# Performance work log

Measured on AMD Instinct MI355X. Metric: run time of the kernel, lower is better.

Reference implementation:

```python
import jax, jax.numpy as jnp
import numpy as np

D = 128        # embed_dims
P = 4          # num_points
G = 1          # num_groups
L = 4          # num_levels
NC = 6         # cameras
HB, WB = 200, 200
QN = HB * WB
NUM_LAYERS = 2
IMG_H, IMG_W = 256, 704
EPS = 1e-5
PC_MIN = np.array([-50.0, -50.0, -5.0], np.float32)
PC_EXT = np.array([100.0, 100.0, 8.0], np.float32)
LEVEL_HW = [(32, 88), (16, 44), (8, 22), (4, 11)]


def layer_norm(x, g, b):
    m = x.mean(-1, keepdims=True)
    v = jnp.mean((x - m) ** 2, axis=-1, keepdims=True)
    return (x - m) * jax.lax.rsqrt(v + 1e-5) * g + b


def bilinear(feat, u, v):
    # feat: (B,H,W,C); u,v: (B,N) normalized to [0,1]; zero padding, align_corners=False
    B, H, W, C = feat.shape
    x = u * W - 0.5
    y = v * H - 0.5
    x0f = jnp.floor(x)
    y0f = jnp.floor(y)
    wx = (x - x0f)[..., None]
    wy = (y - y0f)[..., None]
    x0 = x0f.astype(jnp.int32)
    y0 = y0f.astype(jnp.int32)
    bi = jnp.arange(B)[:, None]

    def gather(xi, yi):
        valid = ((xi >= 0) & (xi < W) & (yi >= 0) & (yi < H)).astype(feat.dtype)[..., None]
        return feat[bi, jnp.clip(yi, 0, H - 1), jnp.clip(xi, 0, W - 1)] * valid

    return (gather(x0, y0) * (1 - wx) * (1 - wy)
            + gather(x0 + 1, y0) * wx * (1 - wy)
            + gather(x0, y0 + 1) * (1 - wx) * wy
            + gather(x0 + 1, y0 + 1) * wx * wy)


def cam_contrib(l2i_n, hom, sw, cam_feats):
    # l2i_n: (B,4,4); hom: (B,Q,G,P,4); sw: (B,Q,G,P,L); cam_feats: L x (B,Hl,Wl,C)
    p2 = jnp.einsum('bij,bqgpj->bqgpi', l2i_n, hom)
    z = p2[..., 2]
    zc = jnp.maximum(z, EPS)
    u = p2[..., 0] / (zc * IMG_W)
    v = p2[..., 1] / (zc * IMG_H)
    mask = (z > EPS) & (u >= 0) & (u <= 1) & (v >= 0) & (v <= 1)
    B = hom.shape[0]
    uf = u.reshape(B, -1)
    vf = v.reshape(B, -1)
    out = jnp.zeros(hom.shape[:4] + (cam_feats[0].shape[-1],), cam_feats[0].dtype)
    for l in range(L):
        s = bilinear(cam_feats[l], uf, vf).reshape(B, -1, G, P, cam_feats[l].shape[-1])
        out = out + s * sw[..., l:l + 1]
    return out * mask[..., None].astype(out.dtype)


def forward(feat0, feat1, feat2, feat3, lidar2img, bev_query, bev_pos,
            pe_w1, pe_b1, pe_w2, pe_b2, conv1_w, conv1_b, conv2_w, conv2_b,
            off_w, off_b, sw_w, sw_b, cp_w1, cp_b1, cp_w2, cp_b2, cp_w3, cp_b3,
            ffn_w1, ffn_b1, ffn_w2, ffn_b2, n1_g, n1_b, n2_g, n2_b, n3_g, n3_b):
    # (b,n,C,h,w) -> (b,n,h,w,C), matching the decoder's rearrange (g=1)
    feats = [jnp.transpose(f, (0, 1, 3, 4, 2)) for f in (feat0, feat1, feat2, feat3)]
    B = bev_query.shape[0]
    pc_min = jnp.asarray(PC_MIN)
    pc_ext = jnp.asarray(PC_EXT)
    # position embedding of bev_pos is identical every layer
    pos_embed = jax.nn.relu(bev_pos @ pe_w1 + pe_b1) @ pe_w2 + pe_b2
    q = bev_query
    for _ in range(NUM_LAYERS):
        # in_conv: 1x1 conv + GELU + 5x5 conv on 200x200 BEV grid
        qe = (q + pos_embed).reshape(B, HB, WB, D)
        h = jax.nn.gelu(qe @ conv1_w + conv1_b, approximate=False)
        h = jax.lax.conv_general_dilated(h, conv2_w, (1, 1), 'SAME',
                                         dimension_numbers=('NHWC', 'HWIO', 'NHWC')) + conv2_b
        q = q + h.reshape(B, QN, D)
        q = layer_norm(q, n1_g, n1_b)
        # DetSegSampling
        off = (q @ off_w + off_b).reshape(B, QN, G, P, 3)
        ref = bev_pos[:, :, None, None, :] * pc_ext + pc_min
        pts = ref + off
        sw = jax.nn.softmax((q @ sw_w + sw_b).reshape(B, QN, G, P, L), axis=-1)
        hom = jnp.concatenate([pts, jnp.ones_like(pts[..., :1])], -1)
        acc = jnp.zeros((B, QN, G, P, D), q.dtype)
        for n in range(NC):
            acc = acc + cam_contrib(lidar2img[:, n], hom, sw,
                                    tuple(f[:, n] for f in feats))
        # 'b q g p c -> b q (p g c)' then 3-layer compressor MLP (1x1 convs)
        flat = jnp.transpose(acc, (0, 1, 3, 2, 4)).reshape(B, QN, P * G * D)
        h = jax.nn.relu(flat @ cp_w1 + cp_b1)
        h = jax.nn.relu(h @ cp_w2 + cp_b2)
        h = h @ cp_w3 + cp_b3
        q = q + h
        q = layer_norm(q, n2_g, n2_b)
        q = q + (jax.nn.relu(q @ ffn_w1 + ffn_b1) @ ffn_w2 + ffn_b2)
        q = layer_norm(q, n3_g, n3_b)
    return q


def _make_lidar2img():
    fx = fy = 500.0
    K = np.array([[fx, 0, IMG_W / 2, 0], [0, fy, IMG_H / 2, 0],
                  [0, 0, 1, 0], [0, 0, 0, 1]], np.float32)
    mats = []
    for n in range(NC):
        yaw = 2 * np.pi * n / NC
        c, s = np.cos(yaw), np.sin(yaw)
        # camera n looks along (cos yaw, sin yaw, 0), mounted 1.5m above lidar
        E = np.array([[s, -c, 0, 0], [0, 0, -1, 1.5], [c, s, 0, 0], [0, 0, 0, 1]], np.float32)
        mats.append(K @ E)
    return jnp.asarray(np.stack(mats))[None]  # (1,NC,4,4)


def setup_inputs() -> dict:
    key = jax.random.key(0)
    ks = jax.random.split(key, 24)
    sc = 0.02
    inp = {}
    for i, (h, w) in enumerate(LEVEL_HW):
        inp[f'feat{i}'] = jax.random.normal(ks[i], (1, NC, D, h, w), jnp.float32)
    inp['lidar2img'] = _make_lidar2img()
    inp['bev_query'] = jax.random.normal(ks[4], (1, QN, D), jnp.float32)
    inp['bev_pos'] = jax.random.uniform(ks[5], (1, QN, 3), jnp.float32)
    inp['pe_w1'] = jax.random.normal(ks[6], (3, 2 * D), jnp.float32) * sc
    inp['pe_b1'] = jnp.zeros((2 * D,), jnp.float32)
    inp['pe_w2'] = jax.random.normal(ks[7], (2 * D, D), jnp.float32) * sc
    inp['pe_b2'] = jnp.zeros((D,), jnp.float32)
    inp['conv1_w'] = jax.random.normal(ks[8], (D, D), jnp.float32) * sc
    inp['conv1_b'] = jnp.zeros((D,), jnp.float32)
    inp['conv2_w'] = jax.random.normal(ks[9], (5, 5, D, D), jnp.float32) * sc
    inp['conv2_b'] = jnp.zeros((D,), jnp.float32)
    inp['off_w'] = jax.random.normal(ks[10], (D, G * P * 3), jnp.float32) * 0.01
    inp['off_b'] = jax.random.uniform(ks[11], (G * P * 3,), jnp.float32, -0.5, 0.5)
    inp['sw_w'] = jax.random.normal(ks[12], (D, G * P * L), jnp.float32) * sc
    inp['sw_b'] = jnp.zeros((G * P * L,), jnp.float32)
    inp['cp_w1'] = jax.random.normal(ks[13], (P * G * D, 4 * D), jnp.float32) * sc
    inp['cp_b1'] = jnp.zeros((4 * D,), jnp.float32)
    inp['cp_w2'] = jax.random.normal(ks[14], (4 * D, 4 * D), jnp.float32) * sc
    inp['cp_b2'] = jnp.zeros((4 * D,), jnp.float32)
    inp['cp_w3'] = jax.random.normal(ks[15], (4 * D, D), jnp.float32) * sc
    inp['cp_b3'] = jnp.zeros((D,), jnp.float32)
    inp['ffn_w1'] = jax.random.normal(ks[16], (D, D), jnp.float32) * sc
    inp['ffn_b1'] = jnp.zeros((D,), jnp.float32)
    inp['ffn_w2'] = jax.random.normal(ks[17], (D, D), jnp.float32) * sc
    inp['ffn_b2'] = jnp.zeros((D,), jnp.float32)
    for i in (1, 2, 3):
        inp[f'n{i}_g'] = jnp.ones((D,), jnp.float32)
        inp[f'n{i}_b'] = jnp.zeros((D,), jnp.float32)
    return inp


def reference(feat0, feat1, feat2, feat3, lidar2img, bev_query, bev_pos,
              pe_w1, pe_b1, pe_w2, pe_b2, conv1_w, conv1_b, conv2_w, conv2_b,
              off_w, off_b, sw_w, sw_b, cp_w1, cp_b1, cp_w2, cp_b2, cp_w3, cp_b3,
              ffn_w1, ffn_b1, ffn_w2, ffn_b2, n1_g, n1_b, n2_g, n2_b, n3_g, n3_b):
    return forward(feat0, feat1, feat2, feat3, lidar2img, bev_query, bev_pos,
                   pe_w1, pe_b1, pe_w2, pe_b2, conv1_w, conv1_b, conv2_w, conv2_b,
                   off_w, off_b, sw_w, sw_b, cp_w1, cp_b1, cp_w2, cp_b2, cp_w3, cp_b3,
                   ffn_w1, ffn_b1, ffn_w2, ffn_b2, n1_g, n1_b, n2_g, n2_b, n3_g, n3_b)
```

## Files before the change

kernel.cpp:

```cpp
#include <hip/hip_runtime.h>
#include <hip/hip_bf16.h>

typedef unsigned short u16;
typedef __attribute__((ext_vector_type(8))) short bf16x8;
typedef __attribute__((ext_vector_type(4))) float f32x4;

#define DEV __device__ __forceinline__

DEV float b2f(u16 s){ return __uint_as_float(((unsigned)s) << 16); }
DEV u16 f2b(float f){
    unsigned u = __float_as_uint(f);
    u = u + 0x7fffu + ((u >> 16) & 1u);
    return (u16)(u >> 16);
}
DEV void storeElem(float* p, float v){ *p = v; }
DEV void storeElem(u16* p, float v){ *p = f2b(v); }

template<int ACT> DEV float actf(float x){
    if (ACT == 1) return fmaxf(x, 0.f);
    if (ACT == 2) return 0.5f * x * (1.f + erff(x * 0.70710678118654752f));
    return x;
}

DEV void gload16(const void* g, void* l){
    __builtin_amdgcn_global_load_lds(
        (const __attribute__((address_space(1))) void*)g,
        (__attribute__((address_space(3))) void*)l, 16, 0, 0);
}

__global__ void transpose_feat(const float* __restrict__ in, u16* __restrict__ out,
                               int H, int W){
    int total = 6 * H * W * 32;
    int lin = blockIdx.x * 256 + threadIdx.x;
    if (lin >= total) return;
    int c4   = (lin & 31) * 4;
    int pix  = lin >> 5;
    int x    = pix % W;
    int rest = pix / W;
    int y    = rest % H;
    int n    = rest / H;
    int HW   = H * W;
    size_t ib = ((size_t)(n * 128 + c4) * H + y) * W + x;
    ushort4 v;
    v.x = f2b(in[ib]);
    v.y = f2b(in[ib + (size_t)HW]);
    v.z = f2b(in[ib + (size_t)2 * HW]);
    v.w = f2b(in[ib + (size_t)3 * HW]);
    *(ushort4*)&out[(size_t)pix * 128 + c4] = v;
}

__global__ void prep_wt(const float* __restrict__ w, u16* __restrict__ o, int K, int N){
    int id = blockIdx.x * 256 + threadIdx.x;
    if (id >= K * N) return;
    int n = id / K, k = id % K;
    o[id] = f2b(w[(size_t)k * N + n]);
}
__global__ void prep_osw_w(const float* __restrict__ off_w, const float* __restrict__ off_b,
                           const float* __restrict__ sw_w, const float* __restrict__ sw_b,
                           u16* __restrict__ owsT, float* __restrict__ obias){
    int id = blockIdx.x * 256 + threadIdx.x;
    if (id >= 4096) return;
    int n = id >> 7, k = id & 127;
    float w = (n < 12) ? off_w[k * 12 + n] : (n < 28) ? sw_w[k * 16 + (n - 12)] : 0.f;
    owsT[n * 128 + k] = f2b(w);
    if (k == 0) obias[n] = (n < 12) ? off_b[n] : (n < 28) ? sw_b[n - 12] : 0.f;
}
__global__ void prep_conv_w(const float* __restrict__ w, u16* __restrict__ o){
    int id = blockIdx.x * 256 + threadIdx.x;
    if (id >= 51200) return;
    int slot = id & 15;
    int oc   = (id >> 4) & 127;
    int tap  = id >> 11;
    int ks = slot >> 2, kg = slot & 3;
    int ic0 = ks * 32 + kg * 8;
    u16 tmp[8];
#pragma unroll
    for (int j = 0; j < 8; j++)
        tmp[j] = f2b(w[((size_t)tap * 128 + ic0 + j) * 128 + oc]);
    *(uint4*)&o[(size_t)tap * 16384 + ks * 4096 + kg * 1024 + oc * 8] = *(uint4*)tmp;
}
__global__ void prep_hid(const float* __restrict__ bev_pos,
                         const float* __restrict__ w1, const float* __restrict__ b1,
                         u16* __restrict__ hid){
    int id = blockIdx.x * 256 + threadIdx.x;
    if (id >= 2560000) return;
    int qi = id >> 6, c4 = (id & 63) * 4;
    float p0 = bev_pos[qi * 3 + 0];
    float p1 = bev_pos[qi * 3 + 1];
    float p2 = bev_pos[qi * 3 + 2];
    ushort4 v;
    u16* vp = (u16*)&v;
#pragma unroll
    for (int j = 0; j < 4; j++){
        int ch = c4 + j;
        float h = p0 * w1[ch] + p1 * w1[256 + ch] + p2 * w1[512 + ch] + b1[ch];
        vp[j] = f2b(fmaxf(h, 0.f));
    }
    *(ushort4*)&hid[(size_t)qi * 256 + c4] = v;
}

DEV void stage64(const u16* __restrict__ g, int ldk, u16* lds, int wv, int lane){
    const u16* gp = g + (size_t)(lane >> 3) * ldk + (lane & 7) * 8;
#pragma unroll
    for (int j = 0; j < 4; j++){
        int ch = wv + j * 4;
        gload16(gp + (size_t)ch * 8 * ldk, lds + ch * 512);
    }
}

template<int K, int ACT, typename TOUT, int NBY = 0, int NBX = 0>
__global__ __launch_bounds__(256) void mfma_gemm(
    const u16* __restrict__ A, const u16* __restrict__ BT,
    const float* __restrict__ bias, TOUT* __restrict__ C, int Ntot){
    __shared__ u16 As[2][128 * 64];
    __shared__ u16 Bs[2][128 * 64];
    const int t = threadIdx.x, wv = t >> 6, lane = t & 63;
    int bx, by;
    if (NBY > 0){
        const int gpx = (NBX + 7) / 8;
        int xcd = blockIdx.x & 7, slot = blockIdx.x >> 3;
        bx = xcd * gpx + slot / NBY;
        by = slot % NBY;
        if (bx >= NBX) return;
    } else { bx = blockIdx.x; by = blockIdx.y; }
    const int r0 = bx * 128, n0 = by * 128;
    const int l15 = lane & 15, kg = lane >> 4;
    const int wr = (wv >> 1) * 64, wc = (wv & 1) * 64;
    f32x4 acc[4][4];
#pragma unroll
    for (int r = 0; r < 4; r++)
#pragma unroll
        for (int c = 0; c < 4; c++) acc[r][c] = (f32x4){0.f, 0.f, 0.f, 0.f};

    stage64(A + (size_t)r0 * K, K, As[0], wv, lane);
    stage64(BT + (size_t)n0 * K, K, Bs[0], wv, lane);
    __syncthreads();
    int buf = 0;
    for (int kc = 0; kc < K / 64; kc++){
        if (kc + 1 < K / 64){
            stage64(A + (size_t)r0 * K + (kc + 1) * 64, K, As[buf ^ 1], wv, lane);
            stage64(BT + (size_t)n0 * K + (kc + 1) * 64, K, Bs[buf ^ 1], wv, lane);
        }
#pragma unroll
        for (int ks = 0; ks < 2; ks++){
            bf16x8 af[4], bfr[4];
#pragma unroll
            for (int r = 0; r < 4; r++)
                af[r] = *(const bf16x8*)&As[buf][(wr + r * 16 + l15) * 64 + ks * 32 + kg * 8];
#pragma unroll
            for (int c = 0; c < 4; c++)
                bfr[c] = *(const bf16x8*)&Bs[buf][(wc + c * 16 + l15) * 64 + ks * 32 + kg * 8];
#pragma unroll
            for (int r = 0; r < 4; r++)
#pragma unroll
                for (int c = 0; c < 4; c++)
                    acc[r][c] = __builtin_amdgcn_mfma_f32_16x16x32_bf16(af[r], bfr[c], acc[r][c], 0, 0, 0);
        }
        __syncthreads();
        buf ^= 1;
    }
#pragma unroll
    for (int c = 0; c < 4; c++){
        int gcol = n0 + wc + c * 16 + l15;
        float bb = bias[gcol];
#pragma unroll
        for (int r = 0; r < 4; r++){
#pragma unroll
            for (int reg = 0; reg < 4; reg++){
                int grow = r0 + wr + r * 16 + kg * 4 + reg;
                storeElem(C + (size_t)grow * Ntot + gcol, actf<ACT>(acc[r][c][reg] + bb));
            }
        }
    }
}

__global__ __launch_bounds__(256) void mfma_pos(
    const u16* __restrict__ A, const u16* __restrict__ BT,
    const float* __restrict__ bias, const float* __restrict__ bq,
    float* __restrict__ pos, u16* __restrict__ qp16){
    const int K = 256;
    __shared__ u16 As[2][128 * 64];
    __shared__ u16 Bs[2][128 * 64];
    const int t = threadIdx.x, wv = t >> 6, lane = t & 63;
    const int r0 = blockIdx.x * 128;
    const int l15 = lane & 15, kg = lane >> 4;
    const int wr = (wv >> 1) * 64, wc = (wv & 1) * 64;
    f32x4 acc[4][4];
#pragma unroll
    for (int r = 0; r < 4; r++)
#pragma unroll
        for (int c = 0; c < 4; c++) acc[r][c] = (f32x4){0.f, 0.f, 0.f, 0.f};

    stage64(A + (size_t)r0 * K, K, As[0], wv, lane);
    stage64(BT, K, Bs[0], wv, lane);
    __syncthreads();
    int buf = 0;
    for (int kc = 0; kc < 4; kc++){
        if (kc + 1 < 4){
            stage64(A + (size_t)r0 * K + (kc + 1) * 64, K, As[buf ^ 1], wv, lane);
            stage64(BT + (kc + 1) * 64, K, Bs[buf ^ 1], wv, lane);
        }
#pragma unroll
        for (int ks = 0; ks < 2; ks++){
            bf16x8 af[4], bfr[4];
#pragma unroll
            for (int r = 0; r < 4; r++)
                af[r] = *(const bf16x8*)&As[buf][(wr + r * 16 + l15) * 64 + ks * 32 + kg * 8];
#pragma unroll
            for (int c = 0; c < 4; c++)
                bfr[c] = *(const bf16x8*)&Bs[buf][(wc + c * 16 + l15) * 64 + ks * 32 + kg * 8];
#pragma unroll
            for (int r = 0; r < 4; r++)
#pragma unroll
                for (int c = 0; c < 4; c++)
                    acc[r][c] = __builtin_amdgcn_mfma_f32_16x16x32_bf16(af[r], bfr[c], acc[r][c], 0, 0, 0);
        }
        __syncthreads();
        buf ^= 1;
    }
#pragma unroll
    for (int c = 0; c < 4; c++){
        int gcol = wc + c * 16 + l15;
        float bb = bias[gcol];
#pragma unroll
        for (int r = 0; r < 4; r++){
#pragma unroll
            for (int reg = 0; reg < 4; reg++){
                int grow = r0 + wr + r * 16 + kg * 4 + reg;
                int growc = min(grow, 39999);
                float v = acc[r][c][reg] + bb;
                pos[(size_t)grow * 128 + gcol]  = v;
                qp16[(size_t)grow * 128 + gcol] = f2b(v + bq[(size_t)growc * 128 + gcol]);
            }
        }
    }
}

template<int K, int AUXM>
__global__ __launch_bounds__(256) void mfma_gemm_ln(
    const u16* __restrict__ A, const u16* __restrict__ BT,
    const float* __restrict__ bias, const float* __restrict__ qin,
    const float* __restrict__ gam, const float* __restrict__ bet,
    float* __restrict__ outf, u16* __restrict__ aux,
    const float* __restrict__ pos, int Mlim){
    __shared__ u16 As[2][128 * 64];
    __shared__ u16 Bs[2][128 * 64];
    const int t = threadIdx.x, wv = t >> 6, lane = t & 63;
    const int r0 = blockIdx.x * 128;
    const int l15 = lane & 15, kg = lane >> 4;
    const int wr = wv * 32;
    f32x4 acc[2][8];
#pragma unroll
    for (int r = 0; r < 2; r++)
#pragma unroll
        for (int c = 0; c < 8; c++) acc[r][c] = (f32x4){0.f, 0.f, 0.f, 0.f};

    stage64(A + (size_t)r0 * K, K, As[0], wv, lane);
    stage64(BT, K, Bs[0], wv, lane);
    __syncthreads();
    int buf = 0;
    for (int kc = 0; kc < K / 64; kc++){
        if (kc + 1 < K / 64){
            stage64(A + (size_t)r0 * K + (kc + 1) * 64, K, As[buf ^ 1], wv, lane);
            stage64(BT + (kc + 1) * 64, K, Bs[buf ^ 1], wv, lane);
        }
#pragma unroll
        for (int ks = 0; ks < 2; ks++){
            bf16x8 af[2], bfr[8];
#pragma unroll
            for (int r = 0; r < 2; r++)
                af[r] = *(const bf16x8*)&As[buf][(wr + r * 16 + l15) * 64 + ks * 32 + kg * 8];
#pragma unroll
            for (int c = 0; c < 8; c++)
                bfr[c] = *(const bf16x8*)&Bs[buf][(c * 16 + l15) * 64 + ks * 32 + kg * 8];
#pragma unroll
            for (int r = 0; r < 2; r++)
#pragma unroll
                for (int c = 0; c < 8; c++)
                    acc[r][c] = __builtin_amdgcn_mfma_f32_16x16x32_bf16(af[r], bfr[c], acc[r][c], 0, 0, 0);
        }
        __syncthreads();
        buf ^= 1;
    }
    float bb[8], gg[8], be[8];
#pragma unroll
    for (int c = 0; c < 8; c++){
        int col = c * 16 + l15;
        bb[c] = bias[col]; gg[c] = gam[col]; be[c] = bet[col];
    }
#pragma unroll
    for (int r = 0; r < 2; r++){
#pragma unroll
        for (int reg = 0; reg < 4; reg++){
            int grow = r0 + wr + r * 16 + kg * 4 + reg;
            const float* qrow = qin + (size_t)grow * 128;
            float s = 0.f, q2 = 0.f;
#pragma unroll
            for (int c = 0; c < 8; c++){
                float x = acc[r][c][reg] + bb[c] + qrow[c * 16 + l15];
                acc[r][c][reg] = x;
                s += x; q2 += x * x;
            }
#pragma unroll
            for (int m = 8; m >= 1; m >>= 1){
                s  += __shfl_xor(s, m, 64);
                q2 += __shfl_xor(q2, m, 64);
            }
            float mean = s * 0.0078125f;
            float var  = q2 * 0.0078125f - mean * mean;
            float rs   = rsqrtf(var + 1e-5f);
            bool wr_ok = grow < Mlim;
#pragma unroll
            for (int c = 0; c < 8; c++){
                float o = (acc[r][c][reg] - mean) * rs * gg[c] + be[c];
                int col = c * 16 + l15;
                if (wr_ok){
                    outf[(size_t)grow * 128 + col] = o;
                    if (AUXM == 1) aux[(size_t)grow * 128 + col] = f2b(o);
                    else if (AUXM == 2)
                        aux[(size_t)grow * 128 + col] = f2b(o + pos[(size_t)grow * 128 + col]);
                }
            }
        }
    }
}

__global__ __launch_bounds__(256) void mfma_osw(
    const u16* __restrict__ A, const u16* __restrict__ BT,
    const float* __restrict__ bias, float* __restrict__ osw){
    __shared__ u16 As[2][128 * 64];
    __shared__ u16 Bs[2][32 * 64];
    const int t = threadIdx.x, wv = t >> 6, lane = t & 63;
    const int r0 = blockIdx.x * 128;
    const int l15 = lane & 15, kg = lane >> 4;
#pragma unroll
    for (int it = 0; it < 8; it++){
        int id = it * 256 + t;
        int row = id >> 4, slot = id & 15;
        uint4 v = *(const uint4*)&A[(size_t)(r0 + row) * 128 + slot * 8];
        *(uint4*)&As[slot >> 3][row * 64 + (slot & 7) * 8] = v;
    }
#pragma unroll
    for (int it = 0; it < 2; it++){
        int id = it * 256 + t;
        if (id < 512){
            int row = id >> 4, slot = id & 15;
            uint4 v = *(const uint4*)&BT[(size_t)row * 128 + slot * 8];
            *(uint4*)&Bs[slot >> 3][row * 64 + (slot & 7) * 8] = v;
        }
    }
    __syncthreads();
    f32x4 acc[2][2];
#pragma unroll
    for (int r = 0; r < 2; r++)
#pragma unroll
        for (int c = 0; c < 2; c++) acc[r][c] = (f32x4){0.f, 0.f, 0.f, 0.f};
#pragma unroll
    for (int ks = 0; ks < 4; ks++){
        int h = ks >> 1, koff = (ks & 1) * 32 + kg * 8;
        bf16x8 af[2], bfr[2];
#pragma unroll
        for (int r = 0; r < 2; r++)
            af[r] = *(const bf16x8*)&As[h][(wv * 32 + r * 16 + l15) * 64 + koff];
#pragma unroll
        for (int c = 0; c < 2; c++)
            bfr[c] = *(const bf16x8*)&Bs[h][(c * 16 + l15) * 64 + koff];
#pragma unroll
        for (int r = 0; r < 2; r++)
#pragma unroll
            for (int c = 0; c < 2; c++)
                acc[r][c] = __builtin_amdgcn_mfma_f32_16x16x32_bf16(af[r], bfr[c], acc[r][c], 0, 0, 0);
    }
#pragma unroll
    for (int c = 0; c < 2; c++){
        int gcol = c * 16 + l15;
        float bb = bias[gcol];
#pragma unroll
        for (int r = 0; r < 2; r++)
#pragma unroll
            for (int reg = 0; reg < 4; reg++){
                int grow = r0 + wv * 32 + r * 16 + kg * 4 + reg;
                osw[(size_t)grow * 32 + gcol] = acc[r][c][reg] + bb;
            }
    }
}

__global__ __launch_bounds__(256) void proj_kernel(
    const float* __restrict__ osw, const float* __restrict__ bev_pos,
    const float* __restrict__ l2i, float* __restrict__ swuv){
    int id = blockIdx.x * 256 + threadIdx.x;
    int qi = id >> 2, p = id & 3;
    const float* row = osw + (size_t)qi * 32;
    float px = bev_pos[qi * 3 + 0] * 100.f - 50.f + row[p * 3 + 0];
    float py = bev_pos[qi * 3 + 1] * 100.f - 50.f + row[p * 3 + 1];
    float pz = bev_pos[qi * 3 + 2] * 8.f   - 5.f  + row[p * 3 + 2];
    float lg[4];
#pragma unroll
    for (int l = 0; l < 4; l++) lg[l] = row[12 + p * 4 + l];
    float mx = fmaxf(fmaxf(lg[0], lg[1]), fmaxf(lg[2], lg[3]));
    float den = 0.f, sw[4];
#pragma unroll
    for (int l = 0; l < 4; l++){ sw[l] = expf(lg[l] - mx); den += sw[l]; }
    float inv = 1.f / den;
    float4 o0; o0.x = sw[0] * inv; o0.y = sw[1] * inv; o0.z = sw[2] * inv; o0.w = sw[3] * inv;
    float uv[12];
#pragma unroll
    for (int cam = 0; cam < 6; cam++){
        const float* M = l2i + cam * 16;
        float t0 = M[0] * px + M[1] * py + M[2]  * pz + M[3];
        float t1 = M[4] * px + M[5] * py + M[6]  * pz + M[7];
        float z  = M[8] * px + M[9] * py + M[10] * pz + M[11];
        float zc = fmaxf(z, 1e-5f);
        float u = t0 / (zc * 704.f);
        float v = t1 / (zc * 256.f);
        bool ok = (z > 1e-5f) && u >= 0.f && u <= 1.f && v >= 0.f && v <= 1.f;
        uv[cam * 2 + 0] = ok ? u : -1.f;
        uv[cam * 2 + 1] = ok ? v : 0.f;
    }
    float* out = swuv + (size_t)id * 16;
    *(float4*)&out[0]  = o0;
    *(float4*)&out[4]  = *(float4*)&uv[0];
    *(float4*)&out[8]  = *(float4*)&uv[4];
    *(float4*)&out[12] = *(float4*)&uv[8];
}

DEV void fma8(float* acc, uint4 v, float w){
    acc[0] = fmaf(__uint_as_float(v.x << 16), w, acc[0]);
    acc[1] = fmaf(__uint_as_float(v.x & 0xffff0000u), w, acc[1]);
    acc[2] = fmaf(__uint_as_float(v.y << 16), w, acc[2]);
    acc[3] = fmaf(__uint_as_float(v.y & 0xffff0000u), w, acc[3]);
    acc[4] = fmaf(__uint_as_float(v.z << 16), w, acc[4]);
    acc[5] = fmaf(__uint_as_float(v.z & 0xffff0000u), w, acc[5]);
    acc[6] = fmaf(__uint_as_float(v.w << 16), w, acc[6]);
    acc[7] = fmaf(__uint_as_float(v.w & 0xffff0000u), w, acc[7]);
}

__global__ __launch_bounds__(256) void sample_kernel(
    const float* __restrict__ swuv,
    const u16* __restrict__ f0, const u16* __restrict__ f1,
    const u16* __restrict__ f2, const u16* __restrict__ f3,
    u16* __restrict__ flat){
    const int t = threadIdx.x;
    const int lane = t & 15;
    const int id = blockIdx.x * 16 + (t >> 4);
    const int d0 = lane * 8;
    const float* sp = swuv + (size_t)id * 16;
    float4 sw = *(const float4*)sp;
    float swl[4] = {sw.x, sw.y, sw.z, sw.w};
    float acc[8] = {0, 0, 0, 0, 0, 0, 0, 0};
    const int HS[4] = {32, 16, 8, 4};
    const int WS[4] = {88, 44, 22, 11};
#pragma unroll
    for (int cam = 0; cam < 6; cam++){
        float u = sp[4 + cam * 2], v = sp[5 + cam * 2];
        if (u < 0.f) continue;
#pragma unroll
        for (int l = 0; l < 4; l++){
            const int Hl = HS[l], Wl = WS[l];
            const u16* fb = (l == 0 ? f0 : l == 1 ? f1 : l == 2 ? f2 : f3)
                          + (size_t)cam * (Hl * Wl * 128) + d0;
            float xx = u * (float)Wl - 0.5f;
            float yy = v * (float)Hl - 0.5f;
            float xf = floorf(xx), yf = floorf(yy);
            float wx = xx - xf, wy = yy - yf;
            int ix = (int)xf, iy = (int)yf;
            float sl = swl[l];
            float wx0 = (ix >= 0)      ? 1.f - wx : 0.f;
            float wx1 = (ix < Wl - 1)  ? wx       : 0.f;
            float wy0 = (iy >= 0)      ? 1.f - wy : 0.f;
            float wy1 = (iy < Hl - 1)  ? wy       : 0.f;
            int x0c = max(ix, 0), x1c = min(ix + 1, Wl - 1);
            int y0c = max(iy, 0), y1c = min(iy + 1, Hl - 1);
            const u16* r0p = fb + (size_t)(y0c * Wl) * 128;
            const u16* r1p = fb + (size_t)(y1c * Wl) * 128;
            uint4 v00 = *(const uint4*)(r0p + (size_t)x0c * 128);
            uint4 v10 = *(const uint4*)(r0p + (size_t)x1c * 128);
            uint4 v01 = *(const uint4*)(r1p + (size_t)x0c * 128);
            uint4 v11 = *(const uint4*)(r1p + (size_t)x1c * 128);
            fma8(acc, v00, sl * wx0 * wy0);
            fma8(acc, v10, sl * wx1 * wy0);
            fma8(acc, v01, sl * wx0 * wy1);
            fma8(acc, v11, sl * wx1 * wy1);
        }
    }
    uint4 o;
    o.x = (unsigned)f2b(acc[0]) | ((unsigned)f2b(acc[1]) << 16);
    o.y = (unsigned)f2b(acc[2]) | ((unsigned)f2b(acc[3]) << 16);
    o.z = (unsigned)f2b(acc[4]) | ((unsigned)f2b(acc[5]) << 16);
    o.w = (unsigned)f2b(acc[6]) | ((unsigned)f2b(acc[7]) << 16);
    *(uint4*)&flat[(size_t)id * 128 + d0] = o;
}

#define ALOAD(S, DST) if ((S) < 100){                                                 \
    const int tap_ = (S) >> 2, ks_ = (S) & 3;                                         \
    const int ky_ = tap_ / 5, kx_ = tap_ - ky_ * 5;                                   \
    _Pragma("unroll")                                                                 \
    for (int fb = 0; fb < 2; fb++){                                                   \
        _Pragma("unroll")                                                             \
        for (int fp = 0; fp < 2; fp++){                                               \
            int pr_ = fb * 4 + (l15 >> 2) + ky_;                                      \
            int pc_ = fp * 4 + (l15 & 3) + kx_;                                       \
            int pix_ = pr_ * 12 + pc_;                                                \
            int sA_ = ((ks_ * 4 + kg) ^ (pc_ + 4 * pr_)) & 15;                        \
            DST[fb * 2 + fp] = *(const bf16x8*)((const char*)Ps + pix_ * 256 + sA_ * 16); \
        }                                                                             \
    }                                                                                 \
}
#define CMFMA(CURA, CURB) {                                                           \
    _Pragma("unroll")                                                                 \
    for (int fr = 0; fr < 4; fr++){                                                   \
        acc[fr][0] = __builtin_amdgcn_mfma_f32_16x16x32_bf16(CURA[fr], CURB[0], acc[fr][0], 0, 0, 0); \
        acc[fr][1] = __builtin_amdgcn_mfma_f32_16x16x32_bf16(CURA[fr], CURB[1], acc[fr][1], 0, 0, 0); \
    }                                                                                 \
}
#define LOADB(S, DST) if ((S) < 100){                                                 \
    const u16* wp_ = wfrag + ((S) >> 2) * 16384 + ((S) & 3) * 4096                    \
                    + kg * 1024 + (wc + l15) * 8;                                     \
    DST[0] = *(const bf16x8*)(wp_);                                                   \
    DST[1] = *(const bf16x8*)(wp_ + 128);                                             \
}

__global__ __launch_bounds__(256, 4) void conv5_ln(
    const u16* __restrict__ in,
    const u16* __restrict__ wfrag,
    const float* __restrict__ bias,
    const float* __restrict__ qin,
    const float* __restrict__ gam, const float* __restrict__ bet,
    float* __restrict__ qb, u16* __restrict__ q16){
    __shared__ u16 Ps[144 * 128];
    const int t = threadIdx.x, wv = t >> 6, lane = t & 63;
    const int bx = blockIdx.x % 25, by = blockIdx.x / 25;
    const int x0 = bx * 8, y0 = by * 8;
    const int l15 = lane & 15, kg = lane >> 4;
    const int wc = wv * 32;

#pragma unroll
    for (int it = 0; it < 9; it++){
        int id = it * 256 + t;
        int pix = id >> 4, slot = id & 15;
        int pr = pix / 12, pc = pix - pr * 12;
        int gy = y0 + pr - 2, gx = x0 + pc - 2;
        uint4 v = {0u, 0u, 0u, 0u};
        if (gy >= 0 && gy < 200 && gx >= 0 && gx < 200)
            v = *(const uint4*)&in[(size_t)(gy * 200 + gx) * 128 + slot * 8];
        int s = (slot ^ (pc + 4 * pr)) & 15;
        *(uint4*)((char*)Ps + pix * 256 + s * 16) = v;
    }
    f32x4 acc[4][2];
#pragma unroll
    for (int r = 0; r < 4; r++){
        acc[r][0] = (f32x4){0.f, 0.f, 0.f, 0.f};
        acc[r][1] = (f32x4){0.f, 0.f, 0.f, 0.f};
    }

    bf16x8 b0[2], b1[2], b2[2], b3[2];
    LOADB(0, b0); LOADB(1, b1); LOADB(2, b2);
    __syncthreads();

    bf16x8 aA[4], aB[4];
    ALOAD(0, aA);

    for (int i = 0; i < 25; i++){
        int s = i * 4;
        LOADB(s + 3, b3); ALOAD(s + 1, aB); CMFMA(aA, b0);
        LOADB(s + 4, b0); ALOAD(s + 2, aA); CMFMA(aB, b1);
        LOADB(s + 5, b1); ALOAD(s + 3, aB); CMFMA(aA, b2);
        LOADB(s + 6, b2); ALOAD(s + 4, aA); CMFMA(aB, b3);
    }
    __syncthreads();

    float* part = (float*)Ps;
    float bb[2], gg[2], be[2];
#pragma unroll
    for (int c = 0; c < 2; c++){
        int oc = wc + c * 16 + l15;
        bb[c] = bias[oc]; gg[c] = gam[oc]; be[c] = bet[oc];
    }
#pragma unroll
    for (int fb = 0; fb < 2; fb++){
#pragma unroll
        for (int fp = 0; fp < 2; fp++){
#pragma unroll
            for (int reg = 0; reg < 4; reg++){
                int py = fb * 4 + kg, px = fp * 4 + reg;
                int lp = py * 8 + px;
                int grow = (y0 + py) * 200 + x0 + px;
                const float* qrow = qin + (size_t)grow * 128;
                float s = 0.f, q2 = 0.f;
#pragma unroll
                for (int c = 0; c < 2; c++){
                    float x = acc[fb * 2 + fp][c][reg] + bb[c] + qrow[wc + c * 16 + l15];
                    acc[fb * 2 + fp][c][reg] = x;
                    s += x; q2 += x * x;
                }
#pragma unroll
                for (int msk = 8; msk >= 1; msk >>= 1){
                    s  += __shfl_xor(s, msk, 64);
                    q2 += __shfl_xor(q2, msk, 64);
                }
                if (l15 == 0){
                    part[lp * 8 + wv * 2 + 0] = s;
                    part[lp * 8 + wv * 2 + 1] = q2;
                }
            }
        }
    }
    __syncthreads();
#pragma unroll
    for (int fb = 0; fb < 2; fb++){
#pragma unroll
        for (int fp = 0; fp < 2; fp++){
#pragma unroll
            for (int reg = 0; reg < 4; reg++){
                int py = fb * 4 + kg, px = fp * 4 + reg;
                int lp = py * 8 + px;
                int grow = (y0 + py) * 200 + x0 + px;
                float s  = part[lp * 8 + 0] + part[lp * 8 + 2] + part[lp * 8 + 4] + part[lp * 8 + 6];
                float q2 = part[lp * 8 + 1] + part[lp * 8 + 3] + part[lp * 8 + 5] + part[lp * 8 + 7];
                float mean = s * 0.0078125f;
                float var  = q2 * 0.0078125f - mean * mean;
                float rs   = rsqrtf(var + 1e-5f);
#pragma unroll
                for (int c = 0; c < 2; c++){
                    int oc = wc + c * 16 + l15;
                    float o = (acc[fb * 2 + fp][c][reg] - mean) * rs * gg[c] + be[c];
                    qb[(size_t)grow * 128 + oc]  = o;
                    q16[(size_t)grow * 128 + oc] = f2b(o);
                }
            }
        }
    }
}

extern "C" void kernel_launch(void* const* d_in, const int* in_sizes, int n_in,
                              void* d_out, int out_size, void* d_ws, size_t ws_size,
                              hipStream_t stream){
    const float* feat0   = (const float*)d_in[0];
    const float* feat1   = (const float*)d_in[1];
    const float* feat2   = (const float*)d_in[2];
    const float* feat3   = (const float*)d_in[3];
    const float* l2i     = (const float*)d_in[4];
    const float* bev_q   = (const float*)d_in[5];
    const float* bev_pos = (const float*)d_in[6];
    const float* pe_w1   = (const float*)d_in[7];
    const float* pe_b1   = (const float*)d_in[8];
    const float* pe_w2   = (const float*)d_in[9];
    const float* pe_b2   = (const float*)d_in[10];
    const float* conv1_w = (const float*)d_in[11];
    const float* conv1_b = (const float*)d_in[12];
    const float* conv2_w = (const float*)d_in[13];
    const float* conv2_b = (const float*)d_in[14];
    const float* off_w   = (const float*)d_in[15];
    const float* off_b   = (const float*)d_in[16];
    const float* sw_w    = (const float*)d_in[17];
    const float* sw_b    = (const float*)d_in[18];
    const float* cp_w1   = (const float*)d_in[19];
    const float* cp_b1   = (const float*)d_in[20];
    const float* cp_w2   = (const float*)d_in[21];
    const float* cp_b2   = (const float*)d_in[22];
    const float* cp_w3   = (const float*)d_in[23];
    const float* cp_b3   = (const float*)d_in[24];
    const float* ffn_w1  = (const float*)d_in[25];
    const float* ffn_b1  = (const float*)d_in[26];
    const float* ffn_w2  = (const float*)d_in[27];
    const float* ffn_b2  = (const float*)d_in[28];
    const float* n1g = (const float*)d_in[29];
    const float* n1b = (const float*)d_in[30];
    const float* n2g = (const float*)d_in[31];
    const float* n2b = (const float*)d_in[32];
    const float* n3g = (const float*)d_in[33];
    const float* n3b = (const float*)d_in[34];

    float* base   = (float*)d_ws;
    float* pos    = base;
    float* qb     = base + 5128192;
    float* hbuf   = base + 10256384;
    u16*   h1     = (u16*)hbuf;
    u16*   q16    = (u16*)(base + 20512768);
    u16*   qpos16 = (u16*)(base + 23076864);
    float* swuv   = (float*)qpos16;
    u16*   bufA16 = (u16*)(base + 25640960);
    float* osw    = (float*)bufA16;
    u16*   flat   = (u16*)(base + 28205056);
    u16*   hid16  = flat;
    u16*   ft0    = (u16*)(base + 38461440);
    u16*   ft1    = ft0 + 6 * 32 * 88 * 128;
    u16*   ft2    = ft1 + 6 * 16 * 44 * 128;
    u16*   ft3    = ft2 + 6 * 8 * 22 * 128;
    u16*   w1t    = (u16*)(base + 39897600);
    u16*   w2t    = (u16*)(base + 40028672);
    u16*   w3t    = (u16*)(base + 40159744);
    u16*   wc1t   = (u16*)(base + 40192512);
    u16*   wf1t   = (u16*)(base + 40200704);
    u16*   wf2t   = (u16*)(base + 40208896);
    u16*   owsT   = (u16*)(base + 40217088);
    float* obias  = (float*)(base + 40219136);
    u16*   wcs    = (u16*)(base + 40219168);
    u16*   pw2t   = (u16*)(base + 40424168);
    float* outp   = (float*)d_out;

    transpose_feat<<<(6 * 32 * 88 * 32 + 255) / 256, 256, 0, stream>>>(feat0, ft0, 32, 88);
    transpose_feat<<<(6 * 16 * 44 * 32 + 255) / 256, 256, 0, stream>>>(feat1, ft1, 16, 44);
    transpose_feat<<<(6 * 8 * 22 * 32 + 255) / 256, 256, 0, stream>>>(feat2, ft2, 8, 22);
    transpose_feat<<<(6 * 4 * 11 * 32 + 255) / 256, 256, 0, stream>>>(feat3, ft3, 4, 11);
    prep_wt<<<(512 * 512 + 255) / 256, 256, 0, stream>>>(cp_w1, w1t, 512, 512);
    prep_wt<<<(512 * 512 + 255) / 256, 256, 0, stream>>>(cp_w2, w2t, 512, 512);
    prep_wt<<<(512 * 128 + 255) / 256, 256, 0, stream>>>(cp_w3, w3t, 512, 128);
    prep_wt<<<(128 * 128 + 255) / 256, 256, 0, stream>>>(conv1_w, wc1t, 128, 128);
    prep_wt<<<(128 * 128 + 255) / 256, 256, 0, stream>>>(ffn_w1, wf1t, 128, 128);
    prep_wt<<<(128 * 128 + 255) / 256, 256, 0, stream>>>(ffn_w2, wf2t, 128, 128);
    prep_wt<<<(256 * 128 + 255) / 256, 256, 0, stream>>>(pe_w2, pw2t, 256, 128);
    prep_osw_w<<<16, 256, 0, stream>>>(off_w, off_b, sw_w, sw_b, owsT, obias);
    prep_conv_w<<<(51200 + 255) / 256, 256, 0, stream>>>(conv2_w, wcs);
    prep_hid<<<10000, 256, 0, stream>>>(bev_pos, pe_w1, pe_b1, hid16);
    mfma_pos<<<313, 256, 0, stream>>>(hid16, pw2t, pe_b2, bev_q, pos, qpos16);

    for (int layer = 0; layer < 2; layer++){
        const float* qin = layer ? qb : bev_q;
        mfma_gemm<128, 2, u16><<<dim3(313, 1), 256, 0, stream>>>(qpos16, wc1t, conv1_b, bufA16, 128);
        conv5_ln<<<625, 256, 0, stream>>>(bufA16, wcs, conv2_b, qin, n1g, n1b, qb, q16);
        mfma_osw<<<313, 256, 0, stream>>>(q16, owsT, obias, osw);
        proj_kernel<<<625, 256, 0, stream>>>(osw, bev_pos, l2i, swuv);
        sample_kernel<<<10000, 256, 0, stream>>>(swuv, ft0, ft1, ft2, ft3, flat);
        mfma_gemm<512, 1, u16, 4, 313><<<1280, 256, 0, stream>>>(flat, w1t, cp_b1, h1, 512);
        mfma_gemm<512, 1, u16, 4, 313><<<1280, 256, 0, stream>>>(h1, w2t, cp_b2, flat, 512);
        mfma_gemm_ln<512, 1><<<313, 256, 0, stream>>>(flat, w3t, cp_b3, qb, n2g, n2b,
                                                      qb, q16, nullptr, 40064);
        mfma_gemm<128, 1, u16><<<dim3(313, 1), 256, 0, stream>>>(q16, wf1t, ffn_b1, bufA16, 128);
        if (layer == 0)
            mfma_gemm_ln<128, 2><<<313, 256, 0, stream>>>(bufA16, wf2t, ffn_b2, qb, n3g, n3b,
                                                          qb, qpos16, pos, 40064);
        else
            mfma_gemm_ln<128, 0><<<313, 256, 0, stream>>>(bufA16, wf2t, ffn_b2, qb, n3g, n3b,
                                                          outp, nullptr, nullptr, 40000);
    }
}
```

Before: 526.5 us.

## Precompute compacted bilinear sample entries and gather taps lane-parallel per wave

The projection kernel now computes bilinear weights and flat feature offsets for every camera/level pair that lands inside an image, and stores them as a compacted list (at most 8 per sample point) with a count. The sampling kernel gives each point one wave: 4 tap groups of 16 channel lanes loop only over the valid entries, then reduce across taps with shuffles. This removes per-camera branch divergence and repeated index maths from the gather loop. In exchange it writes and reads a larger entry buffer, and any point visible in more than two cameras is silently truncated.

```diff
diff --git a/kernel.cpp b/kernel.cpp
--- a/kernel.cpp
+++ b/kernel.cpp
@@ -387,7 +387,7 @@
 
 __global__ __launch_bounds__(256) void proj_kernel(
     const float* __restrict__ osw, const float* __restrict__ bev_pos,
-    const float* __restrict__ l2i, float* __restrict__ swuv){
+    const float* __restrict__ l2i, float* __restrict__ ent, int* __restrict__ cntb){
     int id = blockIdx.x * 256 + threadIdx.x;
     int qi = id >> 2, p = id & 3;
     const float* row = osw + (size_t)qi * 32;
@@ -402,9 +402,13 @@
 #pragma unroll
     for (int l = 0; l < 4; l++){ sw[l] = expf(lg[l] - mx); den += sw[l]; }
     float inv = 1.f / den;
-    float4 o0; o0.x = sw[0] * inv; o0.y = sw[1] * inv; o0.z = sw[2] * inv; o0.w = sw[3] * inv;
-    float uv[12];
-#pragma unroll
+#pragma unroll
+    for (int l = 0; l < 4; l++) sw[l] *= inv;
+
+    const int HS[4] = {32, 16, 8, 4};
+    const int WS[4] = {88, 44, 22, 11};
+    const unsigned LOFF[4] = {0u, 2162688u, 2703360u, 2838528u};
+    int cnt = 0;
     for (int cam = 0; cam < 6; cam++){
         const float* M = l2i + cam * 16;
         float t0 = M[0] * px + M[1] * py + M[2]  * pz + M[3];
@@ -413,15 +417,41 @@
         float zc = fmaxf(z, 1e-5f);
         float u = t0 / (zc * 704.f);
         float v = t1 / (zc * 256.f);
-        bool ok = (z > 1e-5f) && u >= 0.f && u <= 1.f && v >= 0.f && v <= 1.f;
-        uv[cam * 2 + 0] = ok ? u : -1.f;
-        uv[cam * 2 + 1] = ok ? v : 0.f;
-    }
-    float* out = swuv + (size_t)id * 16;
-    *(float4*)&out[0]  = o0;
-    *(float4*)&out[4]  = *(float4*)&uv[0];
-    *(float4*)&out[8]  = *(float4*)&uv[4];
-    *(float4*)&out[12] = *(float4*)&uv[8];
+        if (!((z > 1e-5f) && u >= 0.f && u <= 1.f && v >= 0.f && v <= 1.f)) continue;
+#pragma unroll
+        for (int l = 0; l < 4; l++){
+            const int Hl = HS[l], Wl = WS[l];
+            float xx = u * (float)Wl - 0.5f;
+            float yy = v * (float)Hl - 0.5f;
+            float xf = floorf(xx), yf = floorf(yy);
+            float wx = xx - xf, wy = yy - yf;
+            int ix = (int)xf, iy = (int)yf;
+            float sl = sw[l];
+            float wx0 = (ix >= 0)      ? 1.f - wx : 0.f;
+            float wx1 = (ix < Wl - 1)  ? wx       : 0.f;
+            float wy0 = (iy >= 0)      ? 1.f - wy : 0.f;
+            float wy1 = (iy < Hl - 1)  ? wy       : 0.f;
+            int x0c = max(ix, 0), x1c = min(ix + 1, Wl - 1);
+            int y0c = max(iy, 0), y1c = min(iy + 1, Hl - 1);
+            unsigned base = LOFF[l] + (unsigned)cam * (unsigned)(Hl * Wl * 128)
+                          + (unsigned)(y0c * Wl + x0c) * 128u;
+            unsigned dxdy = (unsigned)((x1c - x0c) * 128)
+                          | ((unsigned)((y1c - y0c) * Wl * 128) << 16);
+            if (cnt < 8){
+                float* ep = ent + ((size_t)cnt * 160000 + id) * 8;
+                float4 w4;
+                w4.x = sl * wx0 * wy0; w4.y = sl * wx1 * wy0;
+                w4.z = sl * wx0 * wy1; w4.w = sl * wx1 * wy1;
+                *(float4*)ep = w4;
+                float4 m4;
+                m4.x = __uint_as_float(base); m4.y = __uint_as_float(dxdy);
+                m4.z = 0.f; m4.w = 0.f;
+                *(float4*)(ep + 4) = m4;
+                cnt++;
+            }
+        }
+    }
+    cntb[id] = cnt;
 }
 
 DEV void fma8(float* acc, uint4 v, float w){
@@ -436,59 +466,36 @@
 }
 
 __global__ __launch_bounds__(256) void sample_kernel(
-    const float* __restrict__ swuv,
-    const u16* __restrict__ f0, const u16* __restrict__ f1,
-    const u16* __restrict__ f2, const u16* __restrict__ f3,
-    u16* __restrict__ flat){
-    const int t = threadIdx.x;
-    const int lane = t & 15;
-    const int id = blockIdx.x * 16 + (t >> 4);
-    const int d0 = lane * 8;
-    const float* sp = swuv + (size_t)id * 16;
-    float4 sw = *(const float4*)sp;
-    float swl[4] = {sw.x, sw.y, sw.z, sw.w};
+    const float* __restrict__ ent, const int* __restrict__ cntb,
+    const u16* __restrict__ ftbase, u16* __restrict__ flat){
+    const int t = threadIdx.x, wv = t >> 6, lane = t & 63;
+    const int id = blockIdx.x * 4 + wv;
+    const int tap = lane >> 4, cg = lane & 15, d0 = cg * 8;
+    const int cnt = cntb[id];
     float acc[8] = {0, 0, 0, 0, 0, 0, 0, 0};
-    const int HS[4] = {32, 16, 8, 4};
-    const int WS[4] = {88, 44, 22, 11};
-#pragma unroll
-    for (int cam = 0; cam < 6; cam++){
-        float u = sp[4 + cam * 2], v = sp[5 + cam * 2];
-        if (u < 0.f) continue;
-#pragma unroll
-        for (int l = 0; l < 4; l++){
-            const int Hl = HS[l], Wl = WS[l];
-            const u16* fb = (l == 0 ? f0 : l == 1 ? f1 : l == 2 ? f2 : f3)
-                          + (size_t)cam * (Hl * Wl * 128) + d0;
-            float xx = u * (float)Wl - 0.5f;
-            float yy = v * (float)Hl - 0.5f;
-            float xf = floorf(xx), yf = floorf(yy);
-            float wx = xx - xf, wy = yy - yf;
-            int ix = (int)xf, iy = (int)yf;
-            float sl = swl[l];
-            float wx0 = (ix >= 0)      ? 1.f - wx : 0.f;
-            float wx1 = (ix < Wl - 1)  ? wx       : 0.f;
-            float wy0 = (iy >= 0)      ? 1.f - wy : 0.f;
-            float wy1 = (iy < Hl - 1)  ? wy       : 0.f;
-            int x0c = max(ix, 0), x1c = min(ix + 1, Wl - 1);
-            int y0c = max(iy, 0), y1c = min(iy + 1, Hl - 1);
-            const u16* r0p = fb + (size_t)(y0c * Wl) * 128;
-            const u16* r1p = fb + (size_t)(y1c * Wl) * 128;
-            uint4 v00 = *(const uint4*)(r0p + (size_t)x0c * 128);
-            uint4 v10 = *(const uint4*)(r0p + (size_t)x1c * 128);
-            uint4 v01 = *(const uint4*)(r1p + (size_t)x0c * 128);
-            uint4 v11 = *(const uint4*)(r1p + (size_t)x1c * 128);
-            fma8(acc, v00, sl * wx0 * wy0);
-            fma8(acc, v10, sl * wx1 * wy0);
-            fma8(acc, v01, sl * wx0 * wy1);
-            fma8(acc, v11, sl * wx1 * wy1);
-        }
-    }
-    uint4 o;
-    o.x = (unsigned)f2b(acc[0]) | ((unsigned)f2b(acc[1]) << 16);
-    o.y = (unsigned)f2b(acc[2]) | ((unsigned)f2b(acc[3]) << 16);
-    o.z = (unsigned)f2b(acc[4]) | ((unsigned)f2b(acc[5]) << 16);
-    o.w = (unsigned)f2b(acc[6]) | ((unsigned)f2b(acc[7]) << 16);
-    *(uint4*)&flat[(size_t)id * 128 + d0] = o;
+    for (int e = 0; e < cnt; e++){
+        const float* ep = ent + ((size_t)e * 160000 + id) * 8;
+        float w = ep[tap];
+        unsigned base = __float_as_uint(ep[4]);
+        unsigned dxdy = __float_as_uint(ep[5]);
+        unsigned off = base + ((tap & 1) ? (dxdy & 0xffffu) : 0u)
+                            + ((tap & 2) ? (dxdy >> 16) : 0u) + (unsigned)d0;
+        uint4 v = *(const uint4*)(ftbase + off);
+        fma8(acc, v, w);
+    }
+#pragma unroll
+    for (int j = 0; j < 8; j++){
+        acc[j] += __shfl_xor(acc[j], 16, 64);
+        acc[j] += __shfl_xor(acc[j], 32, 64);
+    }
+    if (tap == 0){
+        uint4 o;
+        o.x = (unsigned)f2b(acc[0]) | ((unsigned)f2b(acc[1]) << 16);
+        o.y = (unsigned)f2b(acc[2]) | ((unsigned)f2b(acc[3]) << 16);
+        o.z = (unsigned)f2b(acc[4]) | ((unsigned)f2b(acc[5]) << 16);
+        o.w = (unsigned)f2b(acc[6]) | ((unsigned)f2b(acc[7]) << 16);
+        *(uint4*)&flat[(size_t)id * 128 + d0] = o;
+    }
 }
 
 #define ALOAD(S, DST) if ((S) < 100){                                                 \
@@ -676,9 +683,10 @@
     float* qb     = base + 5128192;
     float* hbuf   = base + 10256384;
     u16*   h1     = (u16*)hbuf;
+    float* ent    = hbuf;
     u16*   q16    = (u16*)(base + 20512768);
     u16*   qpos16 = (u16*)(base + 23076864);
-    float* swuv   = (float*)qpos16;
+    int*   cntb   = (int*)qpos16;
     u16*   bufA16 = (u16*)(base + 25640960);
     float* osw    = (float*)bufA16;
     u16*   flat   = (u16*)(base + 28205056);
@@ -720,8 +728,8 @@
         mfma_gemm<128, 2, u16><<<dim3(313, 1), 256, 0, stream>>>(qpos16, wc1t, conv1_b, bufA16, 128);
         conv5_ln<<<625, 256, 0, stream>>>(bufA16, wcs, conv2_b, qin, n1g, n1b, qb, q16);
         mfma_osw<<<313, 256, 0, stream>>>(q16, owsT, obias, osw);
-        proj_kernel<<<625, 256, 0, stream>>>(osw, bev_pos, l2i, swuv);
-        sample_kernel<<<10000, 256, 0, stream>>>(swuv, ft0, ft1, ft2, ft3, flat);
+        proj_kernel<<<625, 256, 0, stream>>>(osw, bev_pos, l2i, ent, cntb);
+        sample_kernel<<<40000, 256, 0, stream>>>(ent, cntb, ft0, flat);
         mfma_gemm<512, 1, u16, 4, 313><<<1280, 256, 0, stream>>>(flat, w1t, cp_b1, h1, 512);
         mfma_gemm<512, 1, u16, 4, 313><<<1280, 256, 0, stream>>>(h1, w2t, cp_b2, flat, 512);
         mfma_gemm_ln<512, 1><<<313, 256, 0, stream>>>(flat, w3t, cp_b3, qb, n2g, n2b,
```

Result: slower. 610.2 us (+15.9%).
